# Kernel optimization log

Hardware: AMD Instinct MI355X
Metric: run time of the kernel (lower is better)

## Reference

```python
import jax, jax.numpy as jnp
import numpy as np

EPS = 1e-06

def elu_feature_map(x):
    return jax.nn.elu(x) + 1.0

def setup_inputs() -> dict:
    key = jax.random.key(0)
    k1, k2, k3 = jax.random.split(key, 3)
    B, N, H, D = 4, 8192, 8, 64
    queries = jax.random.normal(k1, (B, N, H, D), dtype=jnp.float32)
    keys = jax.random.normal(k2, (B, N, H, D), dtype=jnp.float32)
    values = jax.random.normal(k3, (B, N, H, D), dtype=jnp.float32)
    key_lengths_mask = jnp.ones((B, N), dtype=jnp.float32)  # all keys valid
    return {"queries": queries, "keys": keys, "values": values,
            "key_lengths_mask": key_lengths_mask}

def reference(queries, keys, values, key_lengths_mask):
    # queries/keys/values: [B, N, H, D]; key_lengths_mask: [B, N]
    Q = elu_feature_map(queries)
    K = elu_feature_map(keys) * key_lengths_mask[:, :, None, None]
    # KV: [B, H, M, D] outer-product accumulation over sequence
    KV = jnp.einsum('bnhd,bnhm->bhmd', K, values)
    # normalizer Z: [B, N, H]
    Z = 1.0 / (jnp.einsum('bnhd,bhd->bnh', Q, K.sum(axis=1)) + EPS)
    # output V: [B, N, H, M]
    V = jnp.einsum('bnhd,bhmd,bnh->bnhm', Q, KV, Z)
    return V
```

## Files before the change

### kernel.cpp

```cpp
#include <hip/hip_runtime.h>

static constexpr int B = 4;
static constexpr int N = 8192;
static constexpr int H = 8;
static constexpr int BH = B * H;
#define EPSF 1e-6f

typedef _Float16 f16;
typedef _Float16 f16x8 __attribute__((ext_vector_type(8)));
typedef float f32x4 __attribute__((ext_vector_type(4)));

__device__ __forceinline__ float featmap(float x) {
    return x > 0.0f ? (x + 1.0f) : __expf(x);
}

union H8 { f16x8 v; unsigned long long u[2]; };
__device__ __forceinline__ f16x8 lds_load8(const f16* p) {
    H8 r;
    r.u[0] = *(const unsigned long long*)(p);
    r.u[1] = *(const unsigned long long*)(p + 4);
    return r.v;
}
__device__ __forceinline__ unsigned pack2(float a, float b) {
    union { f16 h[2]; unsigned u; } x;
    x.h[0] = (f16)a; x.h[1] = (f16)b;
    return x.u;
}
__device__ __forceinline__ unsigned long long pack4(float a, float b, float c, float d) {
    union { f16 h[4]; unsigned long long u; } x;
    x.h[0] = (f16)a; x.h[1] = (f16)b; x.h[2] = (f16)c; x.h[3] = (f16)d;
    return x.u;
}

static constexpr int S1 = 64;
static constexpr int ROWS1 = N / S1;
static constexpr int NSTEPS1 = ROWS1 / 32;

__global__ __launch_bounds__(256, 2) void kv_pass(
    const float* __restrict__ keys,
    const float* __restrict__ values,
    const float* __restrict__ mask,
    float* __restrict__ kv,
    float* __restrict__ ksum)
{
    const int bh = blockIdx.x, b = bh >> 3, h = bh & 7;
    const int t = threadIdx.x;
    const int wave = t >> 6, lane = t & 63;
    const int p = t >> 4;
    const int c = t & 15;
    const int quad = lane >> 4;
    const int l15 = lane & 15;
    const int n0 = blockIdx.y * ROWS1;

    __shared__ f16 KT[2][64][36];
    __shared__ f16 VT[2][64][36];
    __shared__ float Ksw[4][64];

    const float* mrow = mask + (size_t)b * N;

    int n = n0 + 2 * p;
    size_t g0 = ((size_t)((b * N + n) * H + h)) * 64 + c * 4;
    size_t g1 = g0 + (size_t)H * 64;
    float4 kq0 = *(const float4*)(keys + g0);
    float4 kq1 = *(const float4*)(keys + g1);
    float4 vq0 = *(const float4*)(values + g0);
    float4 vq1 = *(const float4*)(values + g1);
    float mk0 = mrow[n], mk1 = mrow[n + 1];

    f32x4 acc[4];
    #pragma unroll
    for (int i = 0; i < 4; ++i) acc[i] = (f32x4){0.f, 0.f, 0.f, 0.f};
    float ksacc[4] = {0.f, 0.f, 0.f, 0.f};

    for (int s = 0; s < NSTEPS1; ++s) {
        const int buf = s & 1;
        const float fk0[4] = {featmap(kq0.x) * mk0, featmap(kq0.y) * mk0,
                              featmap(kq0.z) * mk0, featmap(kq0.w) * mk0};
        const float fk1[4] = {featmap(kq1.x) * mk1, featmap(kq1.y) * mk1,
                              featmap(kq1.z) * mk1, featmap(kq1.w) * mk1};
        const float fv0[4] = {vq0.x, vq0.y, vq0.z, vq0.w};
        const float fv1[4] = {vq1.x, vq1.y, vq1.z, vq1.w};
        #pragma unroll
        for (int dd = 0; dd < 4; ++dd) {
            ksacc[dd] += fk0[dd] + fk1[dd];
            *(unsigned*)&KT[buf][c * 4 + dd][2 * p] = pack2(fk0[dd], fk1[dd]);
            *(unsigned*)&VT[buf][c * 4 + dd][2 * p] = pack2(fv0[dd], fv1[dd]);
        }
        if (s + 1 < NSTEPS1) {
            const int nn = n0 + (s + 1) * 32 + 2 * p;
            const size_t h0 = ((size_t)((b * N + nn) * H + h)) * 64 + c * 4;
            const size_t h1 = h0 + (size_t)H * 64;
            kq0 = *(const float4*)(keys + h0);
            kq1 = *(const float4*)(keys + h1);
            vq0 = *(const float4*)(values + h0);
            vq1 = *(const float4*)(values + h1);
            mk0 = mrow[nn]; mk1 = mrow[nn + 1];
        }
        __syncthreads();
        const f16x8 afr = lds_load8(&VT[buf][wave * 16 + l15][quad * 8]);
        #pragma unroll
        for (int dt = 0; dt < 4; ++dt) {
            const f16x8 bfr = lds_load8(&KT[buf][dt * 16 + l15][quad * 8]);
            acc[dt] = __builtin_amdgcn_mfma_f32_16x16x32_f16(afr, bfr, acc[dt], 0, 0, 0);
        }
    }

    float* kvb = kv + (size_t)bh * 4096;
    #pragma unroll
    for (int dt = 0; dt < 4; ++dt) {
        #pragma unroll
        for (int reg = 0; reg < 4; ++reg) {
            const int m = wave * 16 + quad * 4 + reg;
            atomicAdd(kvb + m * 64 + dt * 16 + l15, acc[dt][reg]);
        }
    }
    #pragma unroll
    for (int dd = 0; dd < 4; ++dd) {
        float v = ksacc[dd];
        v += __shfl_xor(v, 16);
        v += __shfl_xor(v, 32);
        if (lane < 16) Ksw[wave][lane * 4 + dd] = v;
    }
    __syncthreads();
    if (t < 64) {
        atomicAdd(ksum + bh * 64 + t, Ksw[0][t] + Ksw[1][t] + Ksw[2][t] + Ksw[3][t]);
    }
}

static constexpr int S2 = 64;
static constexpr int ROWS2 = N / S2;

__global__ __launch_bounds__(256, 2) void out_pass(
    const float* __restrict__ queries,
    const float* __restrict__ kv,
    const float* __restrict__ ksum,
    float* __restrict__ out)
{
    const int bh = blockIdx.x, b = bh >> 3, h = bh & 7;
    const int t = threadIdx.x;
    const int wave = t >> 6, lane = t & 63;
    const int quad = lane >> 4;
    const int l15 = lane & 15;
    const int n0 = blockIdx.y * ROWS2;

    __shared__ f16 Qsh[ROWS2][68];
    __shared__ f16 KVh[64][68];
    __shared__ float Ksh[64];

    #pragma unroll
    for (int l = 0; l < 4; ++l) {
        const int idx = t + l * 256;
        const int m = idx >> 4, cc = idx & 15;
        const float4 v = *(const float4*)(kv + (size_t)bh * 4096 + m * 64 + cc * 4);
        *(unsigned long long*)&KVh[m][cc * 4] = pack4(v.x, v.y, v.z, v.w);
    }
    if (t < 64) Ksh[t] = ksum[bh * 64 + t];

    #pragma unroll
    for (int l = 0; l < ROWS2 * 16 / 256; ++l) {
        const int idx = t + l * 256;
        const int r = idx >> 4, cc = idx & 15;
        const int nn = n0 + r;
        const float4 q = *(const float4*)(queries + ((size_t)((b * N + nn) * H + h)) * 64 + cc * 4);
        *(unsigned long long*)&Qsh[r][cc * 4] =
            pack4(featmap(q.x), featmap(q.y), featmap(q.z), featmap(q.w));
    }
    __syncthreads();

    f16x8 bfr[4][2];
    #pragma unroll
    for (int mt = 0; mt < 4; ++mt)
        #pragma unroll
        for (int ks = 0; ks < 2; ++ks)
            bfr[mt][ks] = lds_load8(&KVh[mt * 16 + l15][ks * 32 + quad * 8]);
    f16x8 bz[2];
    #pragma unroll
    for (int ks = 0; ks < 2; ++ks) {
        #pragma unroll
        for (int j = 0; j < 8; ++j) {
            const float kval = Ksh[ks * 32 + quad * 8 + j];
            bz[ks][j] = (l15 == 0) ? (f16)kval : (f16)0.f;
        }
    }

    #pragma unroll
    for (int nt = 0; nt < 2; ++nt) {
        const int r0 = wave * 32 + nt * 16;
        f32x4 acc[4];
        #pragma unroll
        for (int i = 0; i < 4; ++i) acc[i] = (f32x4){0.f, 0.f, 0.f, 0.f};
        f32x4 az = (f32x4){0.f, 0.f, 0.f, 0.f};

        #pragma unroll
        for (int ks = 0; ks < 2; ++ks) {
            const f16x8 afr = lds_load8(&Qsh[r0 + l15][ks * 32 + quad * 8]);
            #pragma unroll
            for (int mt = 0; mt < 4; ++mt)
                acc[mt] = __builtin_amdgcn_mfma_f32_16x16x32_f16(afr, bfr[mt][ks], acc[mt], 0, 0, 0);
            az = __builtin_amdgcn_mfma_f32_16x16x32_f16(afr, bz[ks], az, 0, 0, 0);
        }

        #pragma unroll
        for (int reg = 0; reg < 4; ++reg) {
            const float den = __shfl(az[reg], lane & 48);
            const float zin = 1.0f / (den + EPSF);
            const int nn = n0 + r0 + quad * 4 + reg;
            float* op = out + ((size_t)((b * N + nn) * H + h)) * 64 + l15;
            #pragma unroll
            for (int mt = 0; mt < 4; ++mt)
                op[mt * 16] = acc[mt][reg] * zin;
        }
    }
}

extern "C" void kernel_launch(void* const* d_in, const int* in_sizes, int n_in,
                              void* d_out, int out_size, void* d_ws, size_t ws_size,
                              hipStream_t stream)
{
    const float* q    = (const float*)d_in[0];
    const float* k    = (const float*)d_in[1];
    const float* v    = (const float*)d_in[2];
    const float* mask = (const float*)d_in[3];
    float* out = (float*)d_out;

    float* kv = (float*)d_ws;
    float* ks = kv + (size_t)BH * 64 * 64;

    hipMemsetAsync(d_ws, 0, (size_t)(BH * 64 * 64 + BH * 64) * sizeof(float), stream);
    kv_pass<<<dim3(BH, S1), 256, 0, stream>>>(k, v, mask, kv, ks);
    out_pass<<<dim3(BH, S2), 256, 0, stream>>>(q, kv, ks, out);
}
```

Baseline: 240.2 us.

## Replace global atomics in KV pass with partial buffers and a reduction kernel

The KV accumulation kernel now writes per-split partial KV and key-sum results to a workspace instead of using float atomicAdd. A separate reduce kernel then sums them, which removes the memset and the atomic contention. The split count is halved and the launch bounds occupancy hint is raised. An atomic fallback path is kept for when the workspace is too small. In exchange it adds an extra kernel launch and partial-buffer traffic of about 16MB written and read.

```diff
diff --git a/kernel.cpp b/kernel.cpp
--- a/kernel.cpp
+++ b/kernel.cpp
@@ -32,11 +32,12 @@
     return x.u;
 }
 
-static constexpr int S1 = 64;
+static constexpr int S1 = 32;
 static constexpr int ROWS1 = N / S1;
 static constexpr int NSTEPS1 = ROWS1 / 32;
 
-__global__ __launch_bounds__(256, 2) void kv_pass(
+template<bool ATOMIC>
+__global__ __launch_bounds__(256, 4) void kv_pass(
     const float* __restrict__ keys,
     const float* __restrict__ values,
     const float* __restrict__ mask,
@@ -105,13 +106,15 @@
         }
     }
 
-    float* kvb = kv + (size_t)bh * 4096;
+    float* kvb = ATOMIC ? (kv + (size_t)bh * 4096)
+                        : (kv + ((size_t)blockIdx.y * BH + bh) * 4096);
     #pragma unroll
     for (int dt = 0; dt < 4; ++dt) {
         #pragma unroll
         for (int reg = 0; reg < 4; ++reg) {
             const int m = wave * 16 + quad * 4 + reg;
-            atomicAdd(kvb + m * 64 + dt * 16 + l15, acc[dt][reg]);
+            if (ATOMIC) atomicAdd(kvb + m * 64 + dt * 16 + l15, acc[dt][reg]);
+            else        kvb[m * 64 + dt * 16 + l15] = acc[dt][reg];
         }
     }
     #pragma unroll
@@ -123,7 +126,28 @@
     }
     __syncthreads();
     if (t < 64) {
-        atomicAdd(ksum + bh * 64 + t, Ksw[0][t] + Ksw[1][t] + Ksw[2][t] + Ksw[3][t]);
+        const float s4 = Ksw[0][t] + Ksw[1][t] + Ksw[2][t] + Ksw[3][t];
+        if (ATOMIC) atomicAdd(ksum + bh * 64 + t, s4);
+        else        ksum[((size_t)blockIdx.y * BH + bh) * 64 + t] = s4;
+    }
+}
+
+__global__ __launch_bounds__(256) void reduce_pass(
+    const float* __restrict__ pkv, const float* __restrict__ pks,
+    float* __restrict__ kv, float* __restrict__ ksum)
+{
+    const int idx = blockIdx.x * 256 + threadIdx.x;
+    if (idx < BH * 4096) {
+        float s = 0.f;
+        #pragma unroll 8
+        for (int j = 0; j < S1; ++j) s += pkv[(size_t)j * (BH * 4096) + idx];
+        kv[idx] = s;
+    } else if (idx < BH * 4096 + BH * 64) {
+        const int k = idx - BH * 4096;
+        float s = 0.f;
+        #pragma unroll 8
+        for (int j = 0; j < S1; ++j) s += pks[(size_t)j * (BH * 64) + k];
+        ksum[k] = s;
     }
 }
 
@@ -223,10 +247,25 @@
     const float* mask = (const float*)d_in[3];
     float* out = (float*)d_out;
 
-    float* kv = (float*)d_ws;
-    float* ks = kv + (size_t)BH * 64 * 64;
-
-    hipMemsetAsync(d_ws, 0, (size_t)(BH * 64 * 64 + BH * 64) * sizeof(float), stream);
-    kv_pass<<<dim3(BH, S1), 256, 0, stream>>>(k, v, mask, kv, ks);
-    out_pass<<<dim3(BH, S2), 256, 0, stream>>>(q, kv, ks, out);
-}
+    const size_t PKV = (size_t)S1 * BH * 4096;
+    const size_t PKS = (size_t)S1 * BH * 64;
+    const size_t FIN = (size_t)BH * 4096 + BH * 64;
+    const size_t need = (PKV + PKS + FIN) * sizeof(float);
+
+    if (ws_size >= need) {
+        float* pkv = (float*)d_ws;
+        float* pks = pkv + PKV;
+        float* kvf = pks + PKS;
+        float* ksf = kvf + (size_t)BH * 4096;
+        kv_pass<false><<<dim3(BH, S1), 256, 0, stream>>>(k, v, mask, pkv, pks);
+        const int redElems = BH * 4096 + BH * 64;
+        reduce_pass<<<dim3((redElems + 255) / 256), 256, 0, stream>>>(pkv, pks, kvf, ksf);
+        out_pass<<<dim3(BH, S2), 256, 0, stream>>>(q, kvf, ksf, out);
+    } else {
+        float* kvf = (float*)d_ws;
+        float* ksf = kvf + (size_t)BH * 4096;
+        hipMemsetAsync(d_ws, 0, FIN * sizeof(float), stream);
+        kv_pass<true><<<dim3(BH, S1), 256, 0, stream>>>(k, v, mask, kvf, ksf);
+        out_pass<<<dim3(BH, S2), 256, 0, stream>>>(q, kvf, ksf, out);
+    }
+}
```

Measured after the change: 239.7 us. No clear change (-0.2%).
